# Kernel tuning notes

Measured on AMD Instinct MI355X. Metric: run time of the kernel, lower is better.

The kernel has to match this reference:

```python
import jax, jax.numpy as jnp
import numpy as np

N = 100000      # nodes
E = 1600000     # edges (avg degree 16)
H = 128         # hidden channels
L = 5           # num_layers (only valid range 4<num_layers<8 for this module; 4 index-errors)
ALPHA = 0.1
THETA = 0.5
EPS = 1e-5      # BatchNorm1d default eps


def setup_inputs() -> dict:
    key = jax.random.key(0)
    ks = jax.random.split(key, 8)
    x = jax.random.normal(ks[0], (N, H), dtype=jnp.float32)
    W_in = jax.random.normal(ks[1], (H, H), dtype=jnp.float32) / np.float32(np.sqrt(H))
    b_in = jnp.zeros((H,), jnp.float32)
    conv_W = jax.random.normal(ks[2], (L, H, H), dtype=jnp.float32) / np.float32(np.sqrt(H))
    bn_gamma = jnp.ones((L - 1, H), jnp.float32)
    bn_beta = jnp.zeros((L - 1, H), jnp.float32)
    W_jk = jax.random.normal(ks[3], (4 * H, H), dtype=jnp.float32) / np.float32(np.sqrt(4 * H))
    b_jk = jnp.zeros((H,), jnp.float32)
    src = jax.random.randint(ks[4], (E,), 0, N, dtype=jnp.int32).astype(jnp.int64)
    dst = jax.random.randint(ks[5], (E,), 0, N, dtype=jnp.int32).astype(jnp.int64)
    return dict(x=x, W_in=W_in, b_in=b_in, conv_W=conv_W, bn_gamma=bn_gamma,
                bn_beta=bn_beta, W_jk=W_jk, b_jk=b_jk, src=src, dst=dst)


def _batchnorm(z, gamma, beta):
    # BatchNorm1d, training-mode batch statistics over the node dimension
    m = z.mean(axis=0)
    v = z.var(axis=0)
    return (z - m) * jax.lax.rsqrt(v + EPS) * gamma + beta


def reference(x, W_in, b_in, conv_W, bn_gamma, bn_beta, W_jk, b_jk, src, dst):
    # lins[0]
    z = x @ W_in + b_in          # [N, H]
    x0 = z                       # initial residual for GCNII
    zs = []
    for i in range(L):
        # GCN2Conv (shared_weights=True, normalize=False):
        #   msg = A @ z  (sparse propagation over edge list)
        msg = jax.ops.segment_sum(z[src], dst, num_segments=N)   # [N, H]
        h = (1.0 - ALPHA) * msg + ALPHA * x0
        beta_l = float(np.log(THETA / (i + 1) + 1.0))
        z = (1.0 - beta_l) * h + beta_l * (h @ conv_W[i])
        zs.append(z)
        if i % 4 == 3:
            # JumpingKnowledge('cat') over the 4 layer outputs, then lins[-1].
            # (Original code also applies BN here but immediately overwrites z,
            #  so that BN is dead computation and is skipped.)
            z = jnp.concatenate(zs[:4], axis=-1) @ W_jk + b_jk   # [N, H]
        elif i < L - 1:
            z = jax.nn.relu(_batchnorm(z, bn_gamma[i], bn_beta[i]))
    return z
```

## Files before the change

### kernel.cpp

```cpp
#include <hip/hip_runtime.h>
#include <hip/hip_bf16.h>
#include <cmath>
#include <cstddef>

#define NN 100000
#define HH 128
#define EE 1600000
#define NH (NN * HH)
#define ALPHA_C 0.1f
#define THETA_C 0.5f
#define EPS_C 1e-5f

constexpr int TR = 64;
constexpr int AST = 68;
constexpr int SCAN_B = 256;
constexpr int NBLK = (NN + SCAN_B - 1) / SCAN_B;

__global__ __launch_bounds__(256) void zero_int_k(int* __restrict__ p, int n) {
    int i = blockIdx.x * 256 + threadIdx.x;
    if (i < n) p[i] = 0;
}
__global__ __launch_bounds__(256) void zero_f4_k(float4* __restrict__ p, int n4) {
    int i = blockIdx.x * 256 + threadIdx.x;
    if (i < n4) p[i] = float4{0.f, 0.f, 0.f, 0.f};
}

__global__ void detect_idx64(const int* __restrict__ p, int* __restrict__ flag) {
    int any = 0;
    for (int i = 0; i < 64; ++i) any |= p[2 * i + 1];
    *flag = (any == 0) ? 1 : 0;
}

__device__ __forceinline__ int load_idx(const void* p, int e, int is64) {
    return is64 ? (int)((const long long*)p)[e] : ((const int*)p)[e];
}

__global__ __launch_bounds__(256) void hist_k(
    const void* __restrict__ dstp, const int* __restrict__ flag,
    int* __restrict__ hist)
{
    int e = blockIdx.x * 256 + threadIdx.x;
    if (e >= EE) return;
    atomicAdd(&hist[load_idx(dstp, e, *flag)], 1);
}

__global__ __launch_bounds__(SCAN_B) void scan1_k(
    const int* __restrict__ hist, int* __restrict__ incl, int* __restrict__ bsum)
{
    __shared__ int sh[SCAN_B];
    int t = threadIdx.x;
    int i = blockIdx.x * SCAN_B + t;
    int v = (i < NN) ? hist[i] : 0;
    sh[t] = v;
    __syncthreads();
    for (int off = 1; off < SCAN_B; off <<= 1) {
        int x = (t >= off) ? sh[t - off] : 0;
        __syncthreads();
        sh[t] += x;
        __syncthreads();
    }
    if (i < NN) incl[i] = sh[t];
    if (t == SCAN_B - 1) bsum[blockIdx.x] = sh[t];
}

__global__ __launch_bounds__(512) void scan2_k(int* __restrict__ bsum) {
    __shared__ int sh[512];
    int t = threadIdx.x;
    sh[t] = (t < NBLK) ? bsum[t] : 0;
    __syncthreads();
    for (int off = 1; off < 512; off <<= 1) {
        int x = (t >= off) ? sh[t - off] : 0;
        __syncthreads();
        sh[t] += x;
        __syncthreads();
    }
    if (t < NBLK) bsum[t] = sh[t];
}

__global__ __launch_bounds__(SCAN_B) void scan3_k(
    const int* __restrict__ hist, const int* __restrict__ incl,
    const int* __restrict__ bsum, int* __restrict__ row_ptr,
    int* __restrict__ cursor)
{
    int b = blockIdx.x;
    int i = b * SCAN_B + threadIdx.x;
    if (i < NN) {
        int ex = incl[i] - hist[i] + (b > 0 ? bsum[b - 1] : 0);
        row_ptr[i] = ex;
        cursor[i] = ex;
    }
    if (i == 0) row_ptr[NN] = EE;
}

__global__ __launch_bounds__(256) void fill_k(
    const void* __restrict__ srcp, const void* __restrict__ dstp,
    const int* __restrict__ flag, int* __restrict__ cursor,
    int* __restrict__ sorted_src)
{
    int e = blockIdx.x * 256 + threadIdx.x;
    if (e >= EE) return;
    int is64 = *flag;
    int d = load_idx(dstp, e, is64);
    int pos = atomicAdd(&cursor[d], 1);
    sorted_src[pos] = load_idx(srcp, e, is64);
}

__global__ __launch_bounds__(256) void gather_k(
    const float* __restrict__ z, const int* __restrict__ row_ptr,
    const int* __restrict__ sorted_src,
    const float* __restrict__ stats,
    const float* __restrict__ gamma, const float* __restrict__ beta,
    float* __restrict__ msg)
{
    int node = blockIdx.x * 4 + (threadIdx.x >> 6);
    if (node >= NN) return;
    int lane = threadIdx.x & 63;
    int half = lane >> 5;
    int c4 = lane & 31;

    const bool bn = (stats != nullptr);
    float4 sc = {1.f, 1.f, 1.f, 1.f}, sh = {0.f, 0.f, 0.f, 0.f};
    if (bn) {
        const float invN = 1.f / (float)NN;
        float4 s  = ((const float4*)stats)[c4];
        float4 s2 = ((const float4*)(stats + 128))[c4];
        float4 g  = ((const float4*)gamma)[c4];
        float4 b  = ((const float4*)beta)[c4];
        float m, var;
        m = s.x * invN; var = s2.x * invN - m * m;
        sc.x = rsqrtf(var + EPS_C) * g.x; sh.x = b.x - m * sc.x;
        m = s.y * invN; var = s2.y * invN - m * m;
        sc.y = rsqrtf(var + EPS_C) * g.y; sh.y = b.y - m * sc.y;
        m = s.z * invN; var = s2.z * invN - m * m;
        sc.z = rsqrtf(var + EPS_C) * g.z; sh.z = b.z - m * sc.z;
        m = s.w * invN; var = s2.w * invN - m * m;
        sc.w = rsqrtf(var + EPS_C) * g.w; sh.w = b.w - m * sc.w;
    }

    int e0 = row_ptr[node], e1 = row_ptr[node + 1];
    float4 acc = {0.f, 0.f, 0.f, 0.f};
    for (int e = e0 + half; e < e1; e += 2) {
        int s = sorted_src[e];
        float4 v = ((const float4*)(z + (size_t)s * HH))[c4];
        if (bn) {
            v.x = fmaxf(0.f, v.x * sc.x + sh.x);
            v.y = fmaxf(0.f, v.y * sc.y + sh.y);
            v.z = fmaxf(0.f, v.z * sc.z + sh.z);
            v.w = fmaxf(0.f, v.w * sc.w + sh.w);
        }
        acc.x += v.x; acc.y += v.y; acc.z += v.z; acc.w += v.w;
    }
    acc.x += __shfl_down(acc.x, 32);
    acc.y += __shfl_down(acc.y, 32);
    acc.z += __shfl_down(acc.z, 32);
    acc.w += __shfl_down(acc.w, 32);
    if (half == 0)
        ((float4*)(msg + (size_t)node * HH))[c4] = acc;
}

__global__ __launch_bounds__(256) void prep_w(
    const float* __restrict__ W_in, const float* __restrict__ conv_W,
    float* __restrict__ Wp)
{
    int i = blockIdx.y;
    int idx = blockIdx.x * 256 + threadIdx.x;
    float v;
    if (i == 0) {
        v = W_in[idx];
    } else {
        float bl = logf(THETA_C / (float)i + 1.f);
        int k = idx >> 7, c = idx & 127;
        v = bl * conv_W[(size_t)(i - 1) * 16384 + idx] + ((k == c) ? (1.f - bl) : 0.f);
    }
    Wp[(size_t)i * 16384 + idx] = v;
}

__global__ __launch_bounds__(256, 4) void gemm128(
    const float* __restrict__ src0, const float* __restrict__ src1,
    float cA, float cB, const float* __restrict__ Wp,
    const float* __restrict__ bias, float* __restrict__ out,
    float* __restrict__ statsp, int nrows)
{
    __shared__ float As[HH * AST];
    const int t = threadIdx.x;
    const int tx = t & 31;
    const int ty = t >> 5;
    const int lane = t & 63, w = t >> 6;
    const int row0 = blockIdx.x * TR;
    const bool useB = (cB != 0.f);

#pragma unroll
    for (int i = 0; i < 8; ++i) {
        int r = (i & 3) * 16 + (lane & 15);
        int k4 = ((i >> 2) * 4 + w) * 4 + (lane >> 4);
        float4 v = {0.f, 0.f, 0.f, 0.f};
        if (row0 + r < nrows) {
            float4 a = ((const float4*)(src0 + (size_t)(row0 + r) * HH))[k4];
            if (useB) {
                float4 b = ((const float4*)(src1 + (size_t)(row0 + r) * HH))[k4];
                v.x = cA * a.x + cB * b.x; v.y = cA * a.y + cB * b.y;
                v.z = cA * a.z + cB * b.z; v.w = cA * a.w + cB * b.w;
            } else {
                v.x = cA * a.x; v.y = cA * a.y; v.z = cA * a.z; v.w = cA * a.w;
            }
        }
        int k = k4 * 4;
        As[(k + 0) * AST + r] = v.x;
        As[(k + 1) * AST + r] = v.y;
        As[(k + 2) * AST + r] = v.z;
        As[(k + 3) * AST + r] = v.w;
    }
    __syncthreads();

    float acc[8][4];
#pragma unroll
    for (int ii = 0; ii < 8; ++ii)
#pragma unroll
        for (int j = 0; j < 4; ++j) acc[ii][j] = 0.f;

    const float4* W4 = (const float4*)Wp;
    float4 wbuf[4];
#pragma unroll
    for (int kk = 0; kk < 4; ++kk) wbuf[kk] = W4[kk * 32 + tx];

    for (int k0 = 0; k0 < HH; k0 += 4) {
        float4 wn[4];
        const bool more = (k0 + 4 < HH);
#pragma unroll
        for (int kk = 0; kk < 4; ++kk) {
            if (more) wn[kk] = W4[(k0 + 4 + kk) * 32 + tx];
            int k = k0 + kk;
            const float* ap = &As[k * AST + ty * 8];
            float4 a0 = *(const float4*)ap;
            float4 a1 = *(const float4*)(ap + 4);
            float a[8] = {a0.x, a0.y, a0.z, a0.w, a1.x, a1.y, a1.z, a1.w};
#pragma unroll
            for (int ii = 0; ii < 8; ++ii) {
                acc[ii][0] += a[ii] * wbuf[kk].x;
                acc[ii][1] += a[ii] * wbuf[kk].y;
                acc[ii][2] += a[ii] * wbuf[kk].z;
                acc[ii][3] += a[ii] * wbuf[kk].w;
            }
        }
        if (more) {
#pragma unroll
            for (int kk = 0; kk < 4; ++kk) wbuf[kk] = wn[kk];
        }
    }

    float4 b4 = {0.f, 0.f, 0.f, 0.f};
    if (bias) b4 = ((const float4*)bias)[tx];
    float cs[4] = {0.f, 0.f, 0.f, 0.f}, cq[4] = {0.f, 0.f, 0.f, 0.f};
    const bool doStats = (statsp != nullptr);
#pragma unroll
    for (int ii = 0; ii < 8; ++ii) {
        int r = row0 + ty * 8 + ii;
        if (r < nrows) {
            float4 v = {acc[ii][0] + b4.x, acc[ii][1] + b4.y,
                        acc[ii][2] + b4.z, acc[ii][3] + b4.w};
            ((float4*)out)[(size_t)r * 32 + tx] = v;
            if (doStats) {
                cs[0] += v.x; cq[0] += v.x * v.x;
                cs[1] += v.y; cq[1] += v.y * v.y;
                cs[2] += v.z; cq[2] += v.z * v.z;
                cs[3] += v.w; cq[3] += v.w * v.w;
            }
        }
    }
    if (doStats) {
        __syncthreads();
        float* red = As;
#pragma unroll
        for (int j = 0; j < 4; ++j) {
            red[ty * 128 + tx * 4 + j] = cs[j];
            red[1024 + ty * 128 + tx * 4 + j] = cq[j];
        }
        __syncthreads();
        if (t < 128) {
            float s = 0.f, q = 0.f;
#pragma unroll
            for (int g = 0; g < 8; ++g) {
                s += red[g * 128 + t];
                q += red[1024 + g * 128 + t];
            }
            atomicAdd(&statsp[t], s);
            atomicAdd(&statsp[128 + t], q);
        }
    }
}

__global__ __launch_bounds__(256, 4) void gemm_jk(
    const float* __restrict__ z0, const float* __restrict__ z1,
    const float* __restrict__ z2, const float* __restrict__ z3,
    const float* __restrict__ Wjk, const float* __restrict__ bjk,
    float* __restrict__ out, int nrows)
{
    __shared__ float As[HH * AST];
    const int t = threadIdx.x;
    const int tx = t & 31;
    const int ty = t >> 5;
    const int lane = t & 63, w = t >> 6;
    const int row0 = blockIdx.x * TR;

    float acc[8][4];
#pragma unroll
    for (int ii = 0; ii < 8; ++ii)
#pragma unroll
        for (int j = 0; j < 4; ++j) acc[ii][j] = 0.f;

    const float* srcs[4] = {z0, z1, z2, z3};
    for (int j = 0; j < 4; ++j) {
        if (j) __syncthreads();
        const float* Z = srcs[j];
#pragma unroll
        for (int i = 0; i < 8; ++i) {
            int r = (i & 3) * 16 + (lane & 15);
            int k4 = ((i >> 2) * 4 + w) * 4 + (lane >> 4);
            float4 v = {0.f, 0.f, 0.f, 0.f};
            if (row0 + r < nrows)
                v = ((const float4*)(Z + (size_t)(row0 + r) * HH))[k4];
            int k = k4 * 4;
            As[(k + 0) * AST + r] = v.x;
            As[(k + 1) * AST + r] = v.y;
            As[(k + 2) * AST + r] = v.z;
            As[(k + 3) * AST + r] = v.w;
        }
        __syncthreads();

        const float4* W4 = (const float4*)(Wjk + (size_t)j * 128 * HH);
        float4 wbuf[4];
#pragma unroll
        for (int kk = 0; kk < 4; ++kk) wbuf[kk] = W4[kk * 32 + tx];

        for (int k0 = 0; k0 < HH; k0 += 4) {
            float4 wn[4];
            const bool more = (k0 + 4 < HH);
#pragma unroll
            for (int kk = 0; kk < 4; ++kk) {
                if (more) wn[kk] = W4[(k0 + 4 + kk) * 32 + tx];
                int k = k0 + kk;
                const float* ap = &As[k * AST + ty * 8];
                float4 a0 = *(const float4*)ap;
                float4 a1 = *(const float4*)(ap + 4);
                float a[8] = {a0.x, a0.y, a0.z, a0.w, a1.x, a1.y, a1.z, a1.w};
#pragma unroll
                for (int ii = 0; ii < 8; ++ii) {
                    acc[ii][0] += a[ii] * wbuf[kk].x;
                    acc[ii][1] += a[ii] * wbuf[kk].y;
                    acc[ii][2] += a[ii] * wbuf[kk].z;
                    acc[ii][3] += a[ii] * wbuf[kk].w;
                }
            }
            if (more) {
#pragma unroll
                for (int kk = 0; kk < 4; ++kk) wbuf[kk] = wn[kk];
            }
        }
    }

    float4 b4 = ((const float4*)bjk)[tx];
#pragma unroll
    for (int ii = 0; ii < 8; ++ii) {
        int r = row0 + ty * 8 + ii;
        if (r < nrows) {
            float4 v = {acc[ii][0] + b4.x, acc[ii][1] + b4.y,
                        acc[ii][2] + b4.z, acc[ii][3] + b4.w};
            ((float4*)out)[(size_t)r * 32 + tx] = v;
        }
    }
}

extern "C" void kernel_launch(void* const* d_in, const int* in_sizes, int n_in,
                              void* d_out, int out_size, void* d_ws, size_t ws_size,
                              hipStream_t stream)
{
    const float* x       = (const float*)d_in[0];
    const float* W_in    = (const float*)d_in[1];
    const float* b_in    = (const float*)d_in[2];
    const float* conv_W  = (const float*)d_in[3];
    const float* bn_g    = (const float*)d_in[4];
    const float* bn_b    = (const float*)d_in[5];
    const float* W_jk    = (const float*)d_in[6];
    const float* b_jk    = (const float*)d_in[7];
    const void*  srcp    = d_in[8];
    const void*  dstp    = d_in[9];

    float* ws     = (float*)d_ws;
    float* x0     = ws;
    float* msg    = ws + (size_t)NH;
    float* zs0    = ws + 2 * (size_t)NH;
    float* zs1    = ws + 3 * (size_t)NH;
    float* zs2    = ws + 4 * (size_t)NH;
    float* stats3 = ws + 5 * (size_t)NH;
    int*   flag       = (int*)(stats3 + 768);
    int*   hist       = flag + 1;
    int*   incl       = hist + NN;
    int*   row_ptr    = incl + NN;
    int*   cursor     = row_ptr + NN + 1;
    int*   bsum       = cursor + NN;
    int*   sorted_src = bsum + NBLK + 1;
    float* Wp         = (float*)(sorted_src + EE);

    const int GEMM_GRID = (NN + TR - 1) / TR;
    const int EDGE_GRID = (EE + 255) / 256;
    const int NODE_GRID = (NN + 3) / 4;

    detect_idx64<<<1, 1, 0, stream>>>((const int*)srcp, flag);
    zero_int_k<<<(NN + 255) / 256, 256, 0, stream>>>(hist, NN);
    zero_f4_k<<<1, 192, 0, stream>>>((float4*)stats3, 192);
    hist_k<<<EDGE_GRID, 256, 0, stream>>>(dstp, flag, hist);
    scan1_k<<<NBLK, SCAN_B, 0, stream>>>(hist, incl, bsum);
    scan2_k<<<1, 512, 0, stream>>>(bsum);
    scan3_k<<<NBLK, SCAN_B, 0, stream>>>(hist, incl, bsum, row_ptr, cursor);
    fill_k<<<EDGE_GRID, 256, 0, stream>>>(srcp, dstp, flag, cursor, sorted_src);
    prep_w<<<dim3(64, 6), 256, 0, stream>>>(W_in, conv_W, Wp);

    gemm128<<<GEMM_GRID, 256, 0, stream>>>(x, x, 1.f, 0.f, Wp, b_in, x0,
                                           nullptr, NN);

    const float* act = x0;
    const float* stats_cur = nullptr;
    const float* g_cur = nullptr;
    const float* b_cur = nullptr;

    for (int i = 0; i < 5; ++i) {
        gather_k<<<NODE_GRID, 256, 0, stream>>>(act, row_ptr, sorted_src,
                                                stats_cur, g_cur, b_cur, msg);

        float* zraw = (i >= 3) ? (float*)d_out : (zs0 + (size_t)i * NH);
        float* stats_next = (i < 3) ? (stats3 + (size_t)i * 256) : nullptr;
        gemm128<<<GEMM_GRID, 256, 0, stream>>>(msg, x0, 1.f - ALPHA_C, ALPHA_C,
                                               Wp + (size_t)(i + 1) * 16384,
                                               nullptr, zraw, stats_next, NN);
        if (i < 3) {
            act = zraw;
            stats_cur = stats_next;
            g_cur = bn_g + (size_t)i * HH;
            b_cur = bn_b + (size_t)i * HH;
        } else if (i == 3) {
            gemm_jk<<<GEMM_GRID, 256, 0, stream>>>(zs0, zs1, zs2,
                                                   (const float*)d_out, W_jk, b_jk,
                                                   zs0, NN);
            act = zs0;
            stats_cur = nullptr;
            g_cur = nullptr;
            b_cur = nullptr;
        }
    }
}
```

Measured before the change: 1.593 ms.

## Replace FP32 FMA GEMMs with split-bf16 MFMA (3-pass) matrix-core GEMMs

Rewrites the node-wise 128x128 GEMMs and the JK GEMM to use bf16 MFMA 16x16x32 instructions. Each FP32 operand is split into high and low bf16 parts, and three products (hh, lh, hl) are accumulated to stay close to FP32 accuracy. Weights are pre-transposed and split once in prep kernels, while activations are split while being staged into LDS. The aim is to move GEMM compute from vector ALUs to matrix cores. In exchange it adds conversion work, and the output stores become scalar per-column writes instead of float4.

```diff
diff --git a/kernel.cpp b/kernel.cpp
--- a/kernel.cpp
+++ b/kernel.cpp
@@ -11,10 +11,23 @@
 #define THETA_C 0.5f
 #define EPS_C 1e-5f
 
-constexpr int TR = 64;
-constexpr int AST = 68;
 constexpr int SCAN_B = 256;
 constexpr int NBLK = (NN + SCAN_B - 1) / SCAN_B;
+constexpr int ABST = 136;
+
+typedef __attribute__((ext_vector_type(8))) short s8v;
+typedef __attribute__((ext_vector_type(4))) float f4v;
+
+#define MFMA16(a, b, c) __builtin_amdgcn_mfma_f32_16x16x32_bf16(a, b, c, 0, 0, 0)
+
+__device__ __forceinline__ unsigned short f2bf(float f) {
+    unsigned u = __float_as_uint(f);
+    u += 0x7fffu + ((u >> 16) & 1u);
+    return (unsigned short)(u >> 16);
+}
+__device__ __forceinline__ float bf2f(unsigned short h) {
+    return __uint_as_float((unsigned)h << 16);
+}
 
 __global__ __launch_bounds__(256) void zero_int_k(int* __restrict__ p, int n) {
     int i = blockIdx.x * 256 + threadIdx.x;
@@ -158,41 +171,58 @@
         ((float4*)(msg + (size_t)node * HH))[c4] = acc;
 }
 
-__global__ __launch_bounds__(256) void prep_w(
+__global__ __launch_bounds__(256) void prep_w_t(
     const float* __restrict__ W_in, const float* __restrict__ conv_W,
-    float* __restrict__ Wp)
+    unsigned short* __restrict__ WtH, unsigned short* __restrict__ WtL)
 {
     int i = blockIdx.y;
     int idx = blockIdx.x * 256 + threadIdx.x;
+    int k = idx >> 7, c = idx & 127;
     float v;
     if (i == 0) {
         v = W_in[idx];
     } else {
         float bl = logf(THETA_C / (float)i + 1.f);
-        int k = idx >> 7, c = idx & 127;
         v = bl * conv_W[(size_t)(i - 1) * 16384 + idx] + ((k == c) ? (1.f - bl) : 0.f);
     }
-    Wp[(size_t)i * 16384 + idx] = v;
-}
-
-__global__ __launch_bounds__(256, 4) void gemm128(
+    unsigned short h = f2bf(v);
+    size_t o = (size_t)i * 16384 + c * 128 + k;
+    WtH[o] = h;
+    WtL[o] = f2bf(v - bf2f(h));
+}
+
+__global__ __launch_bounds__(256) void prep_wjk_t(
+    const float* __restrict__ Wjk,
+    unsigned short* __restrict__ WtH, unsigned short* __restrict__ WtL)
+{
+    int idx = blockIdx.x * 256 + threadIdx.x;
+    int k = idx >> 7, c = idx & 127;
+    float v = Wjk[idx];
+    unsigned short h = f2bf(v);
+    size_t o = (size_t)c * 512 + k;
+    WtH[o] = h;
+    WtL[o] = f2bf(v - bf2f(h));
+}
+
+__global__ __launch_bounds__(256) void gemm128(
     const float* __restrict__ src0, const float* __restrict__ src1,
-    float cA, float cB, const float* __restrict__ Wp,
+    float cA, float cB,
+    const unsigned short* __restrict__ WtH, const unsigned short* __restrict__ WtL,
     const float* __restrict__ bias, float* __restrict__ out,
     float* __restrict__ statsp, int nrows)
 {
-    __shared__ float As[HH * AST];
+    __shared__ __align__(16) unsigned short AsH[64 * ABST];
+    __shared__ __align__(16) unsigned short AsL[64 * ABST];
     const int t = threadIdx.x;
-    const int tx = t & 31;
-    const int ty = t >> 5;
-    const int lane = t & 63, w = t >> 6;
-    const int row0 = blockIdx.x * TR;
+    const int lane = t & 63, wv = t >> 6;
+    const int m = lane & 15, quad = lane >> 4;
+    const int row0 = blockIdx.x * 64;
     const bool useB = (cB != 0.f);
 
 #pragma unroll
     for (int i = 0; i < 8; ++i) {
-        int r = (i & 3) * 16 + (lane & 15);
-        int k4 = ((i >> 2) * 4 + w) * 4 + (lane >> 4);
+        int idx = i * 256 + t;
+        int r = idx >> 5, k4 = idx & 31;
         float4 v = {0.f, 0.f, 0.f, 0.f};
         if (row0 + r < nrows) {
             float4 a = ((const float4*)(src0 + (size_t)(row0 + r) * HH))[k4];
@@ -204,84 +234,76 @@
                 v.x = cA * a.x; v.y = cA * a.y; v.z = cA * a.z; v.w = cA * a.w;
             }
         }
-        int k = k4 * 4;
-        As[(k + 0) * AST + r] = v.x;
-        As[(k + 1) * AST + r] = v.y;
-        As[(k + 2) * AST + r] = v.z;
-        As[(k + 3) * AST + r] = v.w;
+        ushort4 hh, ll;
+        hh.x = f2bf(v.x); ll.x = f2bf(v.x - bf2f(hh.x));
+        hh.y = f2bf(v.y); ll.y = f2bf(v.y - bf2f(hh.y));
+        hh.z = f2bf(v.z); ll.z = f2bf(v.z - bf2f(hh.z));
+        hh.w = f2bf(v.w); ll.w = f2bf(v.w - bf2f(hh.w));
+        *(ushort4*)&AsH[r * ABST + k4 * 4] = hh;
+        *(ushort4*)&AsL[r * ABST + k4 * 4] = ll;
     }
     __syncthreads();
 
-    float acc[8][4];
-#pragma unroll
-    for (int ii = 0; ii < 8; ++ii)
-#pragma unroll
-        for (int j = 0; j < 4; ++j) acc[ii][j] = 0.f;
-
-    const float4* W4 = (const float4*)Wp;
-    float4 wbuf[4];
-#pragma unroll
-    for (int kk = 0; kk < 4; ++kk) wbuf[kk] = W4[kk * 32 + tx];
-
-    for (int k0 = 0; k0 < HH; k0 += 4) {
-        float4 wn[4];
-        const bool more = (k0 + 4 < HH);
-#pragma unroll
-        for (int kk = 0; kk < 4; ++kk) {
-            if (more) wn[kk] = W4[(k0 + 4 + kk) * 32 + tx];
-            int k = k0 + kk;
-            const float* ap = &As[k * AST + ty * 8];
-            float4 a0 = *(const float4*)ap;
-            float4 a1 = *(const float4*)(ap + 4);
-            float a[8] = {a0.x, a0.y, a0.z, a0.w, a1.x, a1.y, a1.z, a1.w};
-#pragma unroll
-            for (int ii = 0; ii < 8; ++ii) {
-                acc[ii][0] += a[ii] * wbuf[kk].x;
-                acc[ii][1] += a[ii] * wbuf[kk].y;
-                acc[ii][2] += a[ii] * wbuf[kk].z;
-                acc[ii][3] += a[ii] * wbuf[kk].w;
+    const s8v* A8h = (const s8v*)AsH;
+    const s8v* A8l = (const s8v*)AsL;
+    const int rl = wv * 16 + m;
+    s8v ah[4], al[4];
+#pragma unroll
+    for (int kc = 0; kc < 4; ++kc) {
+        ah[kc] = A8h[rl * 17 + kc * 4 + quad];
+        al[kc] = A8l[rl * 17 + kc * 4 + quad];
+    }
+
+    const s8v* B8h = (const s8v*)WtH;
+    const s8v* B8l = (const s8v*)WtL;
+
+    f4v acc[8];
+#pragma unroll
+    for (int tt = 0; tt < 8; ++tt) {
+        int c = tt * 16 + m;
+        f4v a = {0.f, 0.f, 0.f, 0.f};
+#pragma unroll
+        for (int kc = 0; kc < 4; ++kc) {
+            s8v bh = B8h[c * 16 + kc * 4 + quad];
+            s8v bl = B8l[c * 16 + kc * 4 + quad];
+            a = MFMA16(ah[kc], bh, a);
+            a = MFMA16(al[kc], bh, a);
+            a = MFMA16(ah[kc], bl, a);
+        }
+        acc[tt] = a;
+    }
+
+    const bool doStats = (statsp != nullptr);
+    __syncthreads();
+    float* redS = (float*)AsH;
+    float* redQ = (float*)AsL;
+#pragma unroll
+    for (int tt = 0; tt < 8; ++tt) {
+        int c = tt * 16 + m;
+        float bb = bias ? bias[c] : 0.f;
+        float s = 0.f, q = 0.f;
+#pragma unroll
+        for (int reg = 0; reg < 4; ++reg) {
+            int r = row0 + wv * 16 + quad * 4 + reg;
+            if (r < nrows) {
+                float v = acc[tt][reg] + bb;
+                out[(size_t)r * HH + c] = v;
+                s += v; q += v * v;
             }
         }
-        if (more) {
-#pragma unroll
-            for (int kk = 0; kk < 4; ++kk) wbuf[kk] = wn[kk];
-        }
-    }
-
-    float4 b4 = {0.f, 0.f, 0.f, 0.f};
-    if (bias) b4 = ((const float4*)bias)[tx];
-    float cs[4] = {0.f, 0.f, 0.f, 0.f}, cq[4] = {0.f, 0.f, 0.f, 0.f};
-    const bool doStats = (statsp != nullptr);
-#pragma unroll
-    for (int ii = 0; ii < 8; ++ii) {
-        int r = row0 + ty * 8 + ii;
-        if (r < nrows) {
-            float4 v = {acc[ii][0] + b4.x, acc[ii][1] + b4.y,
-                        acc[ii][2] + b4.z, acc[ii][3] + b4.w};
-            ((float4*)out)[(size_t)r * 32 + tx] = v;
-            if (doStats) {
-                cs[0] += v.x; cq[0] += v.x * v.x;
-                cs[1] += v.y; cq[1] += v.y * v.y;
-                cs[2] += v.z; cq[2] += v.z * v.z;
-                cs[3] += v.w; cq[3] += v.w * v.w;
-            }
+        if (doStats) {
+            redS[(wv * 4 + quad) * 128 + c] = s;
+            redQ[(wv * 4 + quad) * 128 + c] = q;
         }
     }
     if (doStats) {
-        __syncthreads();
-        float* red = As;
-#pragma unroll
-        for (int j = 0; j < 4; ++j) {
-            red[ty * 128 + tx * 4 + j] = cs[j];
-            red[1024 + ty * 128 + tx * 4 + j] = cq[j];
-        }
         __syncthreads();
         if (t < 128) {
             float s = 0.f, q = 0.f;
 #pragma unroll
-            for (int g = 0; g < 8; ++g) {
-                s += red[g * 128 + t];
-                q += red[1024 + g * 128 + t];
+            for (int g = 0; g < 16; ++g) {
+                s += redS[g * 128 + t];
+                q += redQ[g * 128 + t];
             }
             atomicAdd(&statsp[t], s);
             atomicAdd(&statsp[128 + t], q);
@@ -289,83 +311,81 @@
     }
 }
 
-__global__ __launch_bounds__(256, 4) void gemm_jk(
+__global__ __launch_bounds__(256) void gemm_jk(
     const float* __restrict__ z0, const float* __restrict__ z1,
     const float* __restrict__ z2, const float* __restrict__ z3,
-    const float* __restrict__ Wjk, const float* __restrict__ bjk,
-    float* __restrict__ out, int nrows)
-{
-    __shared__ float As[HH * AST];
+    const unsigned short* __restrict__ WtH, const unsigned short* __restrict__ WtL,
+    const float* __restrict__ bjk, float* __restrict__ out, int nrows)
+{
+    __shared__ __align__(16) unsigned short AsH[64 * ABST];
+    __shared__ __align__(16) unsigned short AsL[64 * ABST];
     const int t = threadIdx.x;
-    const int tx = t & 31;
-    const int ty = t >> 5;
-    const int lane = t & 63, w = t >> 6;
-    const int row0 = blockIdx.x * TR;
-
-    float acc[8][4];
-#pragma unroll
-    for (int ii = 0; ii < 8; ++ii)
-#pragma unroll
-        for (int j = 0; j < 4; ++j) acc[ii][j] = 0.f;
-
+    const int lane = t & 63, wv = t >> 6;
+    const int m = lane & 15, quad = lane >> 4;
+    const int row0 = blockIdx.x * 64;
+
+    f4v acc[8];
+#pragma unroll
+    for (int tt = 0; tt < 8; ++tt) acc[tt] = f4v{0.f, 0.f, 0.f, 0.f};
+
+    const s8v* B8h = (const s8v*)WtH;
+    const s8v* B8l = (const s8v*)WtL;
     const float* srcs[4] = {z0, z1, z2, z3};
+
     for (int j = 0; j < 4; ++j) {
         if (j) __syncthreads();
         const float* Z = srcs[j];
 #pragma unroll
         for (int i = 0; i < 8; ++i) {
-            int r = (i & 3) * 16 + (lane & 15);
-            int k4 = ((i >> 2) * 4 + w) * 4 + (lane >> 4);
+            int idx = i * 256 + t;
+            int r = idx >> 5, k4 = idx & 31;
             float4 v = {0.f, 0.f, 0.f, 0.f};
             if (row0 + r < nrows)
                 v = ((const float4*)(Z + (size_t)(row0 + r) * HH))[k4];
-            int k = k4 * 4;
-            As[(k + 0) * AST + r] = v.x;
-            As[(k + 1) * AST + r] = v.y;
-            As[(k + 2) * AST + r] = v.z;
-            As[(k + 3) * AST + r] = v.w;
-        }
-        __syncthreads();
-
-        const float4* W4 = (const float4*)(Wjk + (size_t)j * 128 * HH);
-        float4 wbuf[4];
-#pragma unroll
-        for (int kk = 0; kk < 4; ++kk) wbuf[kk] = W4[kk * 32 + tx];
-
-        for (int k0 = 0; k0 < HH; k0 += 4) {
-            float4 wn[4];
-            const bool more = (k0 + 4 < HH);
-#pragma unroll
-            for (int kk = 0; kk < 4; ++kk) {
-                if (more) wn[kk] = W4[(k0 + 4 + kk) * 32 + tx];
-                int k = k0 + kk;
-                const float* ap = &As[k * AST + ty * 8];
-                float4 a0 = *(const float4*)ap;
-                float4 a1 = *(const float4*)(ap + 4);
-                float a[8] = {a0.x, a0.y, a0.z, a0.w, a1.x, a1.y, a1.z, a1.w};
-#pragma unroll
-                for (int ii = 0; ii < 8; ++ii) {
-                    acc[ii][0] += a[ii] * wbuf[kk].x;
-                    acc[ii][1] += a[ii] * wbuf[kk].y;
-                    acc[ii][2] += a[ii] * wbuf[kk].z;
-                    acc[ii][3] += a[ii] * wbuf[kk].w;
-                }
+            ushort4 hh, ll;
+            hh.x = f2bf(v.x); ll.x = f2bf(v.x - bf2f(hh.x));
+            hh.y = f2bf(v.y); ll.y = f2bf(v.y - bf2f(hh.y));
+            hh.z = f2bf(v.z); ll.z = f2bf(v.z - bf2f(hh.z));
+            hh.w = f2bf(v.w); ll.w = f2bf(v.w - bf2f(hh.w));
+            *(ushort4*)&AsH[r * ABST + k4 * 4] = hh;
+            *(ushort4*)&AsL[r * ABST + k4 * 4] = ll;
+        }
+        __syncthreads();
+
+        const s8v* A8h = (const s8v*)AsH;
+        const s8v* A8l = (const s8v*)AsL;
+        const int rl = wv * 16 + m;
+        s8v ah[4], al[4];
+#pragma unroll
+        for (int kc = 0; kc < 4; ++kc) {
+            ah[kc] = A8h[rl * 17 + kc * 4 + quad];
+            al[kc] = A8l[rl * 17 + kc * 4 + quad];
+        }
+#pragma unroll
+        for (int tt = 0; tt < 8; ++tt) {
+            int c = tt * 16 + m;
+            f4v a = acc[tt];
+#pragma unroll
+            for (int kc = 0; kc < 4; ++kc) {
+                s8v bh = B8h[c * 64 + j * 16 + kc * 4 + quad];
+                s8v bl = B8l[c * 64 + j * 16 + kc * 4 + quad];
+                a = MFMA16(ah[kc], bh, a);
+                a = MFMA16(al[kc], bh, a);
+                a = MFMA16(ah[kc], bl, a);
             }
-            if (more) {
-#pragma unroll
-                for (int kk = 0; kk < 4; ++kk) wbuf[kk] = wn[kk];
-            }
-        }
-    }
-
-    float4 b4 = ((const float4*)bjk)[tx];
-#pragma unroll
-    for (int ii = 0; ii < 8; ++ii) {
-        int r = row0 + ty * 8 + ii;
-        if (r < nrows) {
-            float4 v = {acc[ii][0] + b4.x, acc[ii][1] + b4.y,
-                        acc[ii][2] + b4.z, acc[ii][3] + b4.w};
-            ((float4*)out)[(size_t)r * 32 + tx] = v;
+            acc[tt] = a;
+        }
+    }
+
+#pragma unroll
+    for (int tt = 0; tt < 8; ++tt) {
+        int c = tt * 16 + m;
+        float bb = bjk[c];
+#pragma unroll
+        for (int reg = 0; reg < 4; ++reg) {
+            int r = row0 + wv * 16 + quad * 4 + reg;
+            if (r < nrows)
+                out[(size_t)r * HH + c] = acc[tt][reg] + bb;
         }
     }
 }
@@ -385,13 +405,16 @@
     const void*  srcp    = d_in[8];
     const void*  dstp    = d_in[9];
 
-    float* ws     = (float*)d_ws;
-    float* x0     = ws;
-    float* msg    = ws + (size_t)NH;
-    float* zs0    = ws + 2 * (size_t)NH;
-    float* zs1    = ws + 3 * (size_t)NH;
-    float* zs2    = ws + 4 * (size_t)NH;
-    float* stats3 = ws + 5 * (size_t)NH;
+    unsigned short* WtH   = (unsigned short*)d_ws;
+    unsigned short* WtL   = WtH + 6 * 16384;
+    unsigned short* WjkTH = WtL + 6 * 16384;
+    unsigned short* WjkTL = WjkTH + 65536;
+    float* x0     = (float*)(WjkTL + 65536);
+    float* msg    = x0 + (size_t)NH;
+    float* zs0    = x0 + 2 * (size_t)NH;
+    float* zs1    = x0 + 3 * (size_t)NH;
+    float* zs2    = x0 + 4 * (size_t)NH;
+    float* stats3 = x0 + 5 * (size_t)NH;
     int*   flag       = (int*)(stats3 + 768);
     int*   hist       = flag + 1;
     int*   incl       = hist + NN;
@@ -399,9 +422,8 @@
     int*   cursor     = row_ptr + NN + 1;
     int*   bsum       = cursor + NN;
     int*   sorted_src = bsum + NBLK + 1;
-    float* Wp         = (float*)(sorted_src + EE);
-
-    const int GEMM_GRID = (NN + TR - 1) / TR;
+
+    const int GEMM_GRID = (NN + 63) / 64;
     const int EDGE_GRID = (EE + 255) / 256;
     const int NODE_GRID = (NN + 3) / 4;
 
@@ -413,10 +435,11 @@
     scan2_k<<<1, 512, 0, stream>>>(bsum);
     scan3_k<<<NBLK, SCAN_B, 0, stream>>>(hist, incl, bsum, row_ptr, cursor);
     fill_k<<<EDGE_GRID, 256, 0, stream>>>(srcp, dstp, flag, cursor, sorted_src);
-    prep_w<<<dim3(64, 6), 256, 0, stream>>>(W_in, conv_W, Wp);
-
-    gemm128<<<GEMM_GRID, 256, 0, stream>>>(x, x, 1.f, 0.f, Wp, b_in, x0,
-                                           nullptr, NN);
+    prep_w_t<<<dim3(64, 6), 256, 0, stream>>>(W_in, conv_W, WtH, WtL);
+    prep_wjk_t<<<256, 256, 0, stream>>>(W_jk, WjkTH, WjkTL);
+
+    gemm128<<<GEMM_GRID, 256, 0, stream>>>(x, x, 1.f, 0.f, WtH, WtL,
+                                           b_in, x0, nullptr, NN);
 
     const float* act = x0;
     const float* stats_cur = nullptr;
@@ -429,9 +452,10 @@
 
         float* zraw = (i >= 3) ? (float*)d_out : (zs0 + (size_t)i * NH);
         float* stats_next = (i < 3) ? (stats3 + (size_t)i * 256) : nullptr;
-        gemm128<<<GEMM_GRID, 256, 0, stream>>>(msg, x0, 1.f - ALPHA_C, ALPHA_C,
-                                               Wp + (size_t)(i + 1) * 16384,
-                                               nullptr, zraw, stats_next, NN);
+        gemm128<<<GEMM_GRID, 256, 0, stream>>>(
+            msg, x0, 1.f - ALPHA_C, ALPHA_C,
+            WtH + (size_t)(i + 1) * 16384, WtL + (size_t)(i + 1) * 16384,
+            nullptr, zraw, stats_next, NN);
         if (i < 3) {
             act = zraw;
             stats_cur = stats_next;
@@ -439,8 +463,8 @@
             b_cur = bn_b + (size_t)i * HH;
         } else if (i == 3) {
             gemm_jk<<<GEMM_GRID, 256, 0, stream>>>(zs0, zs1, zs2,
-                                                   (const float*)d_out, W_jk, b_jk,
-                                                   zs0, NN);
+                                                   (const float*)d_out,
+                                                   WjkTH, WjkTL, b_jk, zs0, NN);
             act = zs0;
             stats_cur = nullptr;
             g_cur = nullptr;
```

Result: slower. 1.679 ms (+5.4%).
